# Kernel tuning notes

Measured on AMD Instinct MI355X. Metric: run time of the kernel, lower is better.

Reference implementation:

```python
import jax, jax.numpy as jnp
import numpy as np

DIM = 1024
B, S = 8, 2048
LN_EPS = 1e-5


def setup_inputs() -> dict:
    key = jax.random.key(0)
    k1, k2, k3 = jax.random.split(key, 3)
    x = jax.random.normal(k1, (B, S, DIM), dtype=jnp.float32)
    # xavier_normal for Linear(dim, 3*dim): std = sqrt(2/(fan_in+fan_out))
    w_qkv = jax.random.normal(k2, (3 * DIM, DIM), dtype=jnp.float32) * np.sqrt(2.0 / (DIM + 3 * DIM))
    w_fc = jax.random.normal(k3, (DIM, DIM), dtype=jnp.float32) * np.sqrt(2.0 / (DIM + DIM))
    b_fc = jnp.zeros((DIM,), dtype=jnp.float32)
    gamma = jnp.ones((DIM,), dtype=jnp.float32)
    beta = jnp.zeros((DIM,), dtype=jnp.float32)
    return {"x": x, "w_qkv": w_qkv, "w_fc": w_fc, "b_fc": b_fc, "gamma": gamma, "beta": beta}


def reference(x, w_qkv, w_fc, b_fc, gamma, beta):
    scaling = DIM ** (-0.5)
    # qkv projection (torch Linear: y = x @ W.T), then chunk into q, k, v
    qkv = jnp.einsum('bsd,ed->bse', x, w_qkv)  # [B, S, 3D]
    q, k, v = jnp.split(qkv, 3, axis=-1)
    # attention scores + softmax over keys
    att = jax.nn.softmax(jnp.einsum('bqd,bkd->bqk', q, k) * scaling, axis=-1)
    # NOTE: faithful to the source einsum 'bqk,bvd->bqd' where k and v are
    # independent summed indices (NOT a standard AV contraction).
    y = jnp.einsum('bqk,bvd->bqd', att, v)
    # fc (dropout is identity in eval mode)
    y = jnp.einsum('bqd,ed->bqe', y, w_fc) + b_fc
    # residual + LayerNorm over last dim
    h = x + y
    mu = jnp.mean(h, axis=-1, keepdims=True)
    var = jnp.var(h, axis=-1, keepdims=True)
    return (h - mu) * jax.lax.rsqrt(var + LN_EPS) * gamma + beta
```

## Files before the change

kernel.cpp:

```cpp
#include <hip/hip_runtime.h>

#define DIM   1024
#define BATCH 8
#define SEQ   2048
#define CHUNKS 64
#define ROWS  (SEQ / CHUNKS)
#define LN_EPS 1e-5f

typedef float v4 __attribute__((ext_vector_type(4)));

__global__ __launch_bounds__(256) void k_partial_colsum(
    const float* __restrict__ x, float* __restrict__ partial) {
  int c = blockIdx.x;
  int b = blockIdx.y;
  int t = threadIdx.x;
  const v4* base =
      (const v4*)(x + ((size_t)b * SEQ + (size_t)c * ROWS) * DIM) + t;
  v4 acc = {0.f, 0.f, 0.f, 0.f};
#pragma unroll 8
  for (int s = 0; s < ROWS; ++s) acc += base[(size_t)s * (DIM / 4)];
  ((v4*)partial)[((size_t)c * BATCH + b) * (DIM / 4) + t] = acc;
}

__global__ __launch_bounds__(256) void k_finish_colsum(
    const float* __restrict__ partial, float* __restrict__ xsum) {
  int i4 = blockIdx.x * 256 + threadIdx.x;
  const v4* p = (const v4*)partial;
  v4 acc = {0.f, 0.f, 0.f, 0.f};
#pragma unroll 8
  for (int c = 0; c < CHUNKS; ++c) acc += p[(size_t)c * BATCH * (DIM / 4) + i4];
  ((v4*)xsum)[i4] = acc;
}

__global__ __launch_bounds__(256) void k_gemv(
    const float* __restrict__ vin, const float* __restrict__ W,
    const float* __restrict__ bias, float* __restrict__ vout) {
  int wave = threadIdx.x >> 6;
  int lane = threadIdx.x & 63;
  int o = blockIdx.x * 4 + wave;
  int b = o >> 10;
  int d = o & (DIM - 1);
  const v4* in4 = (const v4*)(vin + (size_t)b * DIM);
  const v4* w4  = (const v4*)(W + (size_t)d * DIM);
  float acc = 0.f;
#pragma unroll
  for (int j = 0; j < 4; ++j) {
    v4 w = w4[lane + 64 * j];
    v4 i = in4[lane + 64 * j];
    acc += w.x * i.x + w.y * i.y + w.z * i.z + w.w * i.w;
  }
#pragma unroll
  for (int off = 32; off; off >>= 1) acc += __shfl_xor(acc, off, 64);
  if (lane == 0) {
    float r = acc;
    if (bias) r += bias[d];
    vout[o] = r;
  }
}

__global__ __launch_bounds__(256) void k_residual_ln(
    const float* __restrict__ x, const float* __restrict__ z,
    const float* __restrict__ gamma, const float* __restrict__ beta,
    float* __restrict__ out) {
  int wave = threadIdx.x >> 6;
  int lane = threadIdx.x & 63;
  int row = blockIdx.x * 4 + wave;
  int b   = row >> 11;

  const v4* xr = (const v4*)(x + (size_t)row * DIM);
  const v4* zr = (const v4*)(z + (size_t)b * DIM);

  v4 h[4];
  float sum = 0.f, ss = 0.f;
#pragma unroll
  for (int j = 0; j < 4; ++j) {
    v4 xv = xr[lane + 64 * j];
    v4 zv = zr[lane + 64 * j];
    v4 hv = xv + zv;
    h[j] = hv;
    sum += hv.x + hv.y + hv.z + hv.w;
    ss  += hv.x * hv.x + hv.y * hv.y + hv.z * hv.z + hv.w * hv.w;
  }
#pragma unroll
  for (int off = 32; off; off >>= 1) {
    sum += __shfl_xor(sum, off, 64);
    ss  += __shfl_xor(ss,  off, 64);
  }

  const float inv = 1.0f / (float)DIM;
  float mu = sum * inv;
  float rs = rsqrtf(ss * inv - mu * mu + LN_EPS);

  v4* outr = (v4*)out + (size_t)row * (DIM / 4);
#pragma unroll
  for (int j = 0; j < 4; ++j) {
    v4 g  = ((const v4*)gamma)[lane + 64 * j];
    v4 be = ((const v4*)beta)[lane + 64 * j];
    v4 o = (h[j] - mu) * rs * g + be;
    __builtin_nontemporal_store(o, &outr[lane + 64 * j]);
  }
}

extern "C" void kernel_launch(void* const* d_in, const int* in_sizes, int n_in,
                              void* d_out, int out_size, void* d_ws, size_t ws_size,
                              hipStream_t stream) {
  const float* x     = (const float*)d_in[0];
  const float* w_qkv = (const float*)d_in[1];
  const float* w_fc  = (const float*)d_in[2];
  const float* b_fc  = (const float*)d_in[3];
  const float* gamma = (const float*)d_in[4];
  const float* beta  = (const float*)d_in[5];
  float* out = (float*)d_out;

  float* ws      = (float*)d_ws;
  float* partial = ws;
  float* xsum    = partial + (size_t)CHUNKS * BATCH * DIM;
  float* vsum    = xsum + (size_t)BATCH * DIM;
  float* z       = vsum + (size_t)BATCH * DIM;

  const float* w_v = w_qkv + (size_t)2 * DIM * DIM;

  hipLaunchKernelGGL(k_partial_colsum, dim3(CHUNKS, BATCH), dim3(256), 0,
                     stream, x, partial);
  hipLaunchKernelGGL(k_finish_colsum, dim3(BATCH * DIM / 4 / 256), dim3(256),
                     0, stream, partial, xsum);

  hipLaunchKernelGGL(k_gemv, dim3(BATCH * DIM / 4), dim3(256), 0, stream,
                     xsum, w_v, (const float*)nullptr, vsum);
  hipLaunchKernelGGL(k_gemv, dim3(BATCH * DIM / 4), dim3(256), 0, stream,
                     vsum, w_fc, b_fc, z);

  hipLaunchKernelGGL(k_residual_ln, dim3(BATCH * SEQ / 4), dim3(256), 0,
                     stream, x, z, gamma, beta, out);
}
```

Baseline: 48.39 us.

## Fold column-sum finish into first GEMV and restructure GEMV and LayerNorm kernels

Removes the separate finish-colsum kernel by having the first GEMV reduce the 128 partial chunks into shared memory before its dot products. Both GEMVs now use 64 blocks of 1024 threads, with each wave handling 8 output rows, instead of one wave per output. The residual LayerNorm processes 4 rows per wave and caches z, gamma and beta in registers. It also drops nontemporal stores and doubles the number of colsum chunks. This cuts one launch and repeated loads, but the GEMV grids are small: each block redundantly reduces the same partials, and only 64 blocks may underfill the GPU.

New measurement: 55.97 us. 1.16x slower.

```diff
diff --git a/kernel.cpp b/kernel.cpp
--- a/kernel.cpp
+++ b/kernel.cpp
@@ -1,103 +1,188 @@
 #include <hip/hip_runtime.h>
 
-#define DIM   1024
-#define BATCH 8
-#define SEQ   2048
-#define CHUNKS 64
-#define ROWS  (SEQ / CHUNKS)
+#define DIM    1024
+#define BATCH  8
+#define SEQ    2048
+#define CHUNKS 128
+#define ROWS   (SEQ / CHUNKS)
 #define LN_EPS 1e-5f
 
 typedef float v4 __attribute__((ext_vector_type(4)));
 
-__global__ __launch_bounds__(256) void k_partial_colsum(
+__device__ __forceinline__ float dot4(v4 a, v4 b) {
+  return a.x * b.x + a.y * b.y + a.z * b.z + a.w * b.w;
+}
+
+__device__ __forceinline__ float wred(float a) {
+#pragma unroll
+  for (int m = 32; m; m >>= 1) a += __shfl_xor(a, m, 64);
+  return a;
+}
+
+__global__ __launch_bounds__(256, 4) void k_partial_colsum(
     const float* __restrict__ x, float* __restrict__ partial) {
-  int c = blockIdx.x;
-  int b = blockIdx.y;
-  int t = threadIdx.x;
-  const v4* base =
-      (const v4*)(x + ((size_t)b * SEQ + (size_t)c * ROWS) * DIM) + t;
-  v4 acc = {0.f, 0.f, 0.f, 0.f};
+  const int blk = blockIdx.x;
+  const int b = blk >> 7, c = blk & (CHUNKS - 1), t = threadIdx.x;
+  const v4* base = (const v4*)x + ((size_t)(b * SEQ + c * ROWS) << 8) + t;
+  v4 a0 = {0.f, 0.f, 0.f, 0.f}, a1 = {0.f, 0.f, 0.f, 0.f};
+#pragma unroll
+  for (int s = 0; s < ROWS; s += 2) {
+    a0 += base[(size_t)s << 8];
+    a1 += base[(size_t)(s + 1) << 8];
+  }
+  ((v4*)partial)[((size_t)(c * BATCH + b) << 8) + t] = a0 + a1;
+}
+
+__global__ __launch_bounds__(1024) void k_gemv1(
+    const float* __restrict__ partial, const float* __restrict__ w_v,
+    float* __restrict__ vsum) {
+  __shared__ v4 ps[4][256];
+  __shared__ float xs[DIM];
+  const int b = blockIdx.x >> 3, sl = blockIdx.x & 7;
+  const int t = threadIdx.x, wv = t >> 6, lane = t & 63;
+  {
+    const int e4 = t & 255, q = t >> 8;
+    const v4* p = (const v4*)partial + ((size_t)b << 8) + e4;
+    v4 acc = {0.f, 0.f, 0.f, 0.f};
 #pragma unroll 8
-  for (int s = 0; s < ROWS; ++s) acc += base[(size_t)s * (DIM / 4)];
-  ((v4*)partial)[((size_t)c * BATCH + b) * (DIM / 4) + t] = acc;
-}
-
-__global__ __launch_bounds__(256) void k_finish_colsum(
-    const float* __restrict__ partial, float* __restrict__ xsum) {
-  int i4 = blockIdx.x * 256 + threadIdx.x;
-  const v4* p = (const v4*)partial;
-  v4 acc = {0.f, 0.f, 0.f, 0.f};
-#pragma unroll 8
-  for (int c = 0; c < CHUNKS; ++c) acc += p[(size_t)c * BATCH * (DIM / 4) + i4];
-  ((v4*)xsum)[i4] = acc;
-}
-
-__global__ __launch_bounds__(256) void k_gemv(
-    const float* __restrict__ vin, const float* __restrict__ W,
-    const float* __restrict__ bias, float* __restrict__ vout) {
-  int wave = threadIdx.x >> 6;
-  int lane = threadIdx.x & 63;
-  int o = blockIdx.x * 4 + wave;
-  int b = o >> 10;
-  int d = o & (DIM - 1);
-  const v4* in4 = (const v4*)(vin + (size_t)b * DIM);
-  const v4* w4  = (const v4*)(W + (size_t)d * DIM);
-  float acc = 0.f;
-#pragma unroll
-  for (int j = 0; j < 4; ++j) {
-    v4 w = w4[lane + 64 * j];
-    v4 i = in4[lane + 64 * j];
-    acc += w.x * i.x + w.y * i.y + w.z * i.z + w.w * i.w;
-  }
-#pragma unroll
-  for (int off = 32; off; off >>= 1) acc += __shfl_xor(acc, off, 64);
-  if (lane == 0) {
-    float r = acc;
-    if (bias) r += bias[d];
-    vout[o] = r;
-  }
-}
-
-__global__ __launch_bounds__(256) void k_residual_ln(
+    for (int k = 0; k < 32; ++k)
+      acc += p[(size_t)(q + 4 * k) * (BATCH * 256)];
+    ps[q][e4] = acc;
+  }
+  __syncthreads();
+  if (t < 256) ((v4*)xs)[t] = ps[0][t] + ps[1][t] + ps[2][t] + ps[3][t];
+  __syncthreads();
+
+  v4 xf[4];
+#pragma unroll
+  for (int j = 0; j < 4; ++j) xf[j] = ((const v4*)xs)[lane + 64 * j];
+
+  const int d0 = sl * 128 + wv * 8;
+#pragma unroll
+  for (int g = 0; g < 2; ++g) {
+    const int d = d0 + g * 4;
+    const v4* r0 = (const v4*)w_v + ((size_t)(d + 0) << 8);
+    const v4* r1 = (const v4*)w_v + ((size_t)(d + 1) << 8);
+    const v4* r2 = (const v4*)w_v + ((size_t)(d + 2) << 8);
+    const v4* r3 = (const v4*)w_v + ((size_t)(d + 3) << 8);
+    v4 w0[4], w1[4], w2[4], w3[4];
+#pragma unroll
+    for (int j = 0; j < 4; ++j) {
+      w0[j] = r0[lane + 64 * j];
+      w1[j] = r1[lane + 64 * j];
+      w2[j] = r2[lane + 64 * j];
+      w3[j] = r3[lane + 64 * j];
+    }
+    float a0 = 0.f, a1 = 0.f, a2 = 0.f, a3 = 0.f;
+#pragma unroll
+    for (int j = 0; j < 4; ++j) {
+      a0 += dot4(w0[j], xf[j]);
+      a1 += dot4(w1[j], xf[j]);
+      a2 += dot4(w2[j], xf[j]);
+      a3 += dot4(w3[j], xf[j]);
+    }
+    a0 = wred(a0); a1 = wred(a1); a2 = wred(a2); a3 = wred(a3);
+    if (lane == 0) {
+      float* vp = vsum + ((size_t)b << 10) + d;
+      vp[0] = a0; vp[1] = a1; vp[2] = a2; vp[3] = a3;
+    }
+  }
+}
+
+__global__ __launch_bounds__(1024) void k_gemv2(
+    const float* __restrict__ vsum, const float* __restrict__ w_fc,
+    const float* __restrict__ b_fc, float* __restrict__ z) {
+  __shared__ float vs[DIM];
+  const int b = blockIdx.x >> 3, sl = blockIdx.x & 7;
+  const int t = threadIdx.x, wv = t >> 6, lane = t & 63;
+  if (t < 256) ((v4*)vs)[t] = ((const v4*)vsum)[((size_t)b << 8) + t];
+  __syncthreads();
+
+  v4 vf[4];
+#pragma unroll
+  for (int j = 0; j < 4; ++j) vf[j] = ((const v4*)vs)[lane + 64 * j];
+
+  const int d0 = sl * 128 + wv * 8;
+#pragma unroll
+  for (int g = 0; g < 2; ++g) {
+    const int d = d0 + g * 4;
+    const v4* r0 = (const v4*)w_fc + ((size_t)(d + 0) << 8);
+    const v4* r1 = (const v4*)w_fc + ((size_t)(d + 1) << 8);
+    const v4* r2 = (const v4*)w_fc + ((size_t)(d + 2) << 8);
+    const v4* r3 = (const v4*)w_fc + ((size_t)(d + 3) << 8);
+    v4 w0[4], w1[4], w2[4], w3[4];
+#pragma unroll
+    for (int j = 0; j < 4; ++j) {
+      w0[j] = r0[lane + 64 * j];
+      w1[j] = r1[lane + 64 * j];
+      w2[j] = r2[lane + 64 * j];
+      w3[j] = r3[lane + 64 * j];
+    }
+    float a0 = 0.f, a1 = 0.f, a2 = 0.f, a3 = 0.f;
+#pragma unroll
+    for (int j = 0; j < 4; ++j) {
+      a0 += dot4(w0[j], vf[j]);
+      a1 += dot4(w1[j], vf[j]);
+      a2 += dot4(w2[j], vf[j]);
+      a3 += dot4(w3[j], vf[j]);
+    }
+    a0 = wred(a0); a1 = wred(a1); a2 = wred(a2); a3 = wred(a3);
+    if (lane == 0) {
+      float* zp = z + ((size_t)b << 10) + d;
+      zp[0] = a0 + b_fc[d];
+      zp[1] = a1 + b_fc[d + 1];
+      zp[2] = a2 + b_fc[d + 2];
+      zp[3] = a3 + b_fc[d + 3];
+    }
+  }
+}
+
+__global__ __launch_bounds__(256, 4) void k_residual_ln(
     const float* __restrict__ x, const float* __restrict__ z,
     const float* __restrict__ gamma, const float* __restrict__ beta,
     float* __restrict__ out) {
-  int wave = threadIdx.x >> 6;
-  int lane = threadIdx.x & 63;
-  int row = blockIdx.x * 4 + wave;
-  int b   = row >> 11;
-
-  const v4* xr = (const v4*)(x + (size_t)row * DIM);
-  const v4* zr = (const v4*)(z + (size_t)b * DIM);
-
-  v4 h[4];
-  float sum = 0.f, ss = 0.f;
+  __shared__ float zl[DIM];
+  const int blk = blockIdx.x, t = threadIdx.x;
+  const int wv = t >> 6, lane = t & 63;
+  const int b = blk >> 7;
+
+  ((v4*)zl)[t] = ((const v4*)z)[((size_t)b << 8) + t];
+  __syncthreads();
+
+  v4 zf[4], gf[4], bf[4];
 #pragma unroll
   for (int j = 0; j < 4; ++j) {
-    v4 xv = xr[lane + 64 * j];
-    v4 zv = zr[lane + 64 * j];
-    v4 hv = xv + zv;
-    h[j] = hv;
-    sum += hv.x + hv.y + hv.z + hv.w;
-    ss  += hv.x * hv.x + hv.y * hv.y + hv.z * hv.z + hv.w * hv.w;
-  }
-#pragma unroll
-  for (int off = 32; off; off >>= 1) {
-    sum += __shfl_xor(sum, off, 64);
-    ss  += __shfl_xor(ss,  off, 64);
-  }
-
-  const float inv = 1.0f / (float)DIM;
-  float mu = sum * inv;
-  float rs = rsqrtf(ss * inv - mu * mu + LN_EPS);
-
-  v4* outr = (v4*)out + (size_t)row * (DIM / 4);
-#pragma unroll
-  for (int j = 0; j < 4; ++j) {
-    v4 g  = ((const v4*)gamma)[lane + 64 * j];
-    v4 be = ((const v4*)beta)[lane + 64 * j];
-    v4 o = (h[j] - mu) * rs * g + be;
-    __builtin_nontemporal_store(o, &outr[lane + 64 * j]);
+    zf[j] = ((const v4*)zl)[lane + 64 * j];
+    gf[j] = ((const v4*)gamma)[lane + 64 * j];
+    bf[j] = ((const v4*)beta)[lane + 64 * j];
+  }
+
+#pragma unroll 1
+  for (int r = 0; r < 4; ++r) {
+    const int row = (blk << 4) + (wv << 2) + r;
+    const v4* xr = (const v4*)x + ((size_t)row << 8);
+    v4 h[4];
+    float sum = 0.f, ss = 0.f;
+#pragma unroll
+    for (int j = 0; j < 4; ++j) {
+      v4 hv = xr[lane + 64 * j] + zf[j];
+      h[j] = hv;
+      sum += hv.x + hv.y + hv.z + hv.w;
+      ss  += hv.x * hv.x + hv.y * hv.y + hv.z * hv.z + hv.w * hv.w;
+    }
+#pragma unroll
+    for (int m = 32; m; m >>= 1) {
+      sum += __shfl_xor(sum, m, 64);
+      ss  += __shfl_xor(ss,  m, 64);
+    }
+    const float inv = 1.0f / (float)DIM;
+    const float mu = sum * inv;
+    const float rs = rsqrtf(ss * inv - mu * mu + LN_EPS);
+
+    v4* outr = (v4*)out + ((size_t)row << 8);
+#pragma unroll
+    for (int j = 0; j < 4; ++j)
+      outr[lane + 64 * j] = (h[j] - mu) * rs * gf[j] + bf[j];
   }
 }
 
@@ -112,24 +197,18 @@
   const float* beta  = (const float*)d_in[5];
   float* out = (float*)d_out;
 
-  float* ws      = (float*)d_ws;
-  float* partial = ws;
-  float* xsum    = partial + (size_t)CHUNKS * BATCH * DIM;
-  float* vsum    = xsum + (size_t)BATCH * DIM;
+  float* partial = (float*)d_ws;
+  float* vsum    = partial + (size_t)CHUNKS * BATCH * DIM;
   float* z       = vsum + (size_t)BATCH * DIM;
 
   const float* w_v = w_qkv + (size_t)2 * DIM * DIM;
 
-  hipLaunchKernelGGL(k_partial_colsum, dim3(CHUNKS, BATCH), dim3(256), 0,
+  hipLaunchKernelGGL(k_partial_colsum, dim3(BATCH * CHUNKS), dim3(256), 0,
                      stream, x, partial);
-  hipLaunchKernelGGL(k_finish_colsum, dim3(BATCH * DIM / 4 / 256), dim3(256),
-                     0, stream, partial, xsum);
-
-  hipLaunchKernelGGL(k_gemv, dim3(BATCH * DIM / 4), dim3(256), 0, stream,
-                     xsum, w_v, (const float*)nullptr, vsum);
-  hipLaunchKernelGGL(k_gemv, dim3(BATCH * DIM / 4), dim3(256), 0, stream,
+  hipLaunchKernelGGL(k_gemv1, dim3(64), dim3(1024), 0, stream,
+                     partial, w_v, vsum);
+  hipLaunchKernelGGL(k_gemv2, dim3(64), dim3(1024), 0, stream,
                      vsum, w_fc, b_fc, z);
-
-  hipLaunchKernelGGL(k_residual_ln, dim3(BATCH * SEQ / 4), dim3(256), 0,
+  hipLaunchKernelGGL(k_residual_ln, dim3(BATCH * SEQ / 16), dim3(256), 0,
                      stream, x, z, gamma, beta, out);
 }
```

## Process four rows per wave in LayerNorm and split colsum finish across lanes

Applied to the files above, without the earlier changes.

The residual LayerNorm kernel now has each wave handle four rows. It stages the per-batch z vector in shared memory and keeps z, gamma and beta in registers, so they are loaded once per block instead of once per row, and the launch count drops by 4x. The finish-colsum kernel spreads the 64 chunk partials over 8 lanes per output with a shuffle reduction, giving 64 blocks instead of 8 for more parallelism. Output stores switch from nontemporal to regular, which may pollute cache, and the partial colsum uses two accumulators with a flattened grid.

Result: faster. 47.15 us (-2.6%).

```diff
diff --git a/kernel.cpp b/kernel.cpp
--- a/kernel.cpp
+++ b/kernel.cpp
@@ -1,56 +1,67 @@
 #include <hip/hip_runtime.h>
 
-#define DIM   1024
-#define BATCH 8
-#define SEQ   2048
+#define DIM    1024
+#define BATCH  8
+#define SEQ    2048
 #define CHUNKS 64
-#define ROWS  (SEQ / CHUNKS)
+#define ROWS   (SEQ / CHUNKS)
 #define LN_EPS 1e-5f
 
 typedef float v4 __attribute__((ext_vector_type(4)));
 
-__global__ __launch_bounds__(256) void k_partial_colsum(
+__device__ __forceinline__ float dot4(v4 a, v4 b) {
+  return a.x * b.x + a.y * b.y + a.z * b.z + a.w * b.w;
+}
+
+__global__ __launch_bounds__(256, 4) void k_partial_colsum(
     const float* __restrict__ x, float* __restrict__ partial) {
-  int c = blockIdx.x;
-  int b = blockIdx.y;
-  int t = threadIdx.x;
-  const v4* base =
-      (const v4*)(x + ((size_t)b * SEQ + (size_t)c * ROWS) * DIM) + t;
-  v4 acc = {0.f, 0.f, 0.f, 0.f};
-#pragma unroll 8
-  for (int s = 0; s < ROWS; ++s) acc += base[(size_t)s * (DIM / 4)];
-  ((v4*)partial)[((size_t)c * BATCH + b) * (DIM / 4) + t] = acc;
+  const int blk = blockIdx.x;
+  const int b = blk >> 6, c = blk & (CHUNKS - 1), t = threadIdx.x;
+  const v4* base = (const v4*)x + ((size_t)(b * SEQ + c * ROWS) << 8) + t;
+  v4 a0 = {0.f, 0.f, 0.f, 0.f}, a1 = {0.f, 0.f, 0.f, 0.f};
+#pragma unroll
+  for (int s = 0; s < ROWS; s += 2) {
+    a0 += base[(size_t)s << 8];
+    a1 += base[(size_t)(s + 1) << 8];
+  }
+  ((v4*)partial)[((size_t)(c * BATCH + b) << 8) + t] = a0 + a1;
 }
 
 __global__ __launch_bounds__(256) void k_finish_colsum(
     const float* __restrict__ partial, float* __restrict__ xsum) {
-  int i4 = blockIdx.x * 256 + threadIdx.x;
-  const v4* p = (const v4*)partial;
+  const int t = threadIdx.x;
+  const int i4 = blockIdx.x * 32 + (t >> 3);
+  const int grp = t & 7;
+  const int b = i4 >> 8, e4 = i4 & 255;
+  const v4* p = (const v4*)partial + ((size_t)b << 8) + e4;
   v4 acc = {0.f, 0.f, 0.f, 0.f};
-#pragma unroll 8
-  for (int c = 0; c < CHUNKS; ++c) acc += p[(size_t)c * BATCH * (DIM / 4) + i4];
-  ((v4*)xsum)[i4] = acc;
+#pragma unroll
+  for (int k = 0; k < 8; ++k)
+    acc += p[(size_t)(grp + 8 * k) * (BATCH * 256)];
+#pragma unroll
+  for (int m = 4; m; m >>= 1) {
+    acc.x += __shfl_xor(acc.x, m, 64);
+    acc.y += __shfl_xor(acc.y, m, 64);
+    acc.z += __shfl_xor(acc.z, m, 64);
+    acc.w += __shfl_xor(acc.w, m, 64);
+  }
+  if (grp == 0) ((v4*)xsum)[i4] = acc;
 }
 
 __global__ __launch_bounds__(256) void k_gemv(
     const float* __restrict__ vin, const float* __restrict__ W,
     const float* __restrict__ bias, float* __restrict__ vout) {
-  int wave = threadIdx.x >> 6;
-  int lane = threadIdx.x & 63;
-  int o = blockIdx.x * 4 + wave;
-  int b = o >> 10;
-  int d = o & (DIM - 1);
-  const v4* in4 = (const v4*)(vin + (size_t)b * DIM);
-  const v4* w4  = (const v4*)(W + (size_t)d * DIM);
+  const int wv = threadIdx.x >> 6, lane = threadIdx.x & 63;
+  const int o = blockIdx.x * 4 + wv;
+  const int b = o >> 10, d = o & (DIM - 1);
+  const v4* in4 = (const v4*)vin + ((size_t)b << 8);
+  const v4* w4  = (const v4*)W + ((size_t)d << 8);
   float acc = 0.f;
 #pragma unroll
-  for (int j = 0; j < 4; ++j) {
-    v4 w = w4[lane + 64 * j];
-    v4 i = in4[lane + 64 * j];
-    acc += w.x * i.x + w.y * i.y + w.z * i.z + w.w * i.w;
-  }
+  for (int j = 0; j < 4; ++j)
+    acc += dot4(w4[lane + 64 * j], in4[lane + 64 * j]);
 #pragma unroll
-  for (int off = 32; off; off >>= 1) acc += __shfl_xor(acc, off, 64);
+  for (int m = 32; m; m >>= 1) acc += __shfl_xor(acc, m, 64);
   if (lane == 0) {
     float r = acc;
     if (bias) r += bias[d];
@@ -58,46 +69,52 @@
   }
 }
 
-__global__ __launch_bounds__(256) void k_residual_ln(
+__global__ __launch_bounds__(256, 4) void k_residual_ln(
     const float* __restrict__ x, const float* __restrict__ z,
     const float* __restrict__ gamma, const float* __restrict__ beta,
     float* __restrict__ out) {
-  int wave = threadIdx.x >> 6;
-  int lane = threadIdx.x & 63;
-  int row = blockIdx.x * 4 + wave;
-  int b   = row >> 11;
+  __shared__ float zl[DIM];
+  const int blk = blockIdx.x, t = threadIdx.x;
+  const int wv = t >> 6, lane = t & 63;
+  const int b = blk >> 7;
 
-  const v4* xr = (const v4*)(x + (size_t)row * DIM);
-  const v4* zr = (const v4*)(z + (size_t)b * DIM);
+  ((v4*)zl)[t] = ((const v4*)z)[((size_t)b << 8) + t];
+  __syncthreads();
 
-  v4 h[4];
-  float sum = 0.f, ss = 0.f;
+  v4 zf[4], gf[4], bf[4];
 #pragma unroll
   for (int j = 0; j < 4; ++j) {
-    v4 xv = xr[lane + 64 * j];
-    v4 zv = zr[lane + 64 * j];
-    v4 hv = xv + zv;
-    h[j] = hv;
-    sum += hv.x + hv.y + hv.z + hv.w;
-    ss  += hv.x * hv.x + hv.y * hv.y + hv.z * hv.z + hv.w * hv.w;
-  }
-#pragma unroll
-  for (int off = 32; off; off >>= 1) {
-    sum += __shfl_xor(sum, off, 64);
-    ss  += __shfl_xor(ss,  off, 64);
+    zf[j] = ((const v4*)zl)[lane + 64 * j];
+    gf[j] = ((const v4*)gamma)[lane + 64 * j];
+    bf[j] = ((const v4*)beta)[lane + 64 * j];
   }
 
-  const float inv = 1.0f / (float)DIM;
-  float mu = sum * inv;
-  float rs = rsqrtf(ss * inv - mu * mu + LN_EPS);
+#pragma unroll 1
+  for (int r = 0; r < 4; ++r) {
+    const int row = (blk << 4) + (wv << 2) + r;
+    const v4* xr = (const v4*)x + ((size_t)row << 8);
+    v4 h[4];
+    float sum = 0.f, ss = 0.f;
+#pragma unroll
+    for (int j = 0; j < 4; ++j) {
+      v4 hv = xr[lane + 64 * j] + zf[j];
+      h[j] = hv;
+      sum += hv.x + hv.y + hv.z + hv.w;
+      ss  += hv.x * hv.x + hv.y * hv.y + hv.z * hv.z + hv.w * hv.w;
+    }
+#pragma unroll
+    for (int m = 32; m; m >>= 1) {
+      sum += __shfl_xor(sum, m, 64);
+      ss  += __shfl_xor(ss,  m, 64);
+    }
+    const float inv = 1.0f / (float)DIM;
+    const float mu = sum * inv;
+    const float rs = rsqrtf(ss * inv - mu * mu + LN_EPS);
 
-  v4* outr = (v4*)out + (size_t)row * (DIM / 4);
+    v4* outr = (v4*)out + ((size_t)row << 8);
 #pragma unroll
-  for (int j = 0; j < 4; ++j) {
-    v4 g  = ((const v4*)gamma)[lane + 64 * j];
-    v4 be = ((const v4*)beta)[lane + 64 * j];
-    v4 o = (h[j] - mu) * rs * g + be;
-    __builtin_nontemporal_store(o, &outr[lane + 64 * j]);
+    for (int j = 0; j < 4; ++j)
+      outr[lane + 64 * j] = (h[j] - mu) * rs * gf[j] + bf[j];
   }
 }
 
@@ -112,24 +129,21 @@
   const float* beta  = (const float*)d_in[5];
   float* out = (float*)d_out;
 
-  float* ws      = (float*)d_ws;
-  float* partial = ws;
+  float* partial = (float*)d_ws;
   float* xsum    = partial + (size_t)CHUNKS * BATCH * DIM;
   float* vsum    = xsum + (size_t)BATCH * DIM;
   float* z       = vsum + (size_t)BATCH * DIM;
 
   const float* w_v = w_qkv + (size_t)2 * DIM * DIM;
 
-  hipLaunchKernelGGL(k_partial_colsum, dim3(CHUNKS, BATCH), dim3(256), 0,
+  hipLaunchKernelGGL(k_partial_colsum, dim3(BATCH * CHUNKS), dim3(256), 0,
                      stream, x, partial);
-  hipLaunchKernelGGL(k_finish_colsum, dim3(BATCH * DIM / 4 / 256), dim3(256),
-                     0, stream, partial, xsum);
-
+  hipLaunchKernelGGL(k_finish_colsum, dim3(64), dim3(256), 0, stream,
+                     partial, xsum);
   hipLaunchKernelGGL(k_gemv, dim3(BATCH * DIM / 4), dim3(256), 0, stream,
                      xsum, w_v, (const float*)nullptr, vsum);
   hipLaunchKernelGGL(k_gemv, dim3(BATCH * DIM / 4), dim3(256), 0, stream,
                      vsum, w_fc, b_fc, z);
-
-  hipLaunchKernelGGL(k_residual_ln, dim3(BATCH * SEQ / 4), dim3(256), 0,
+  hipLaunchKernelGGL(k_residual_ln, dim3(BATCH * SEQ / 16), dim3(256), 0,
                      stream, x, z, gamma, beta, out);
 }
```
